# Kernel optimization log

Hardware: AMD Instinct MI355X
Metric: run time of the kernel (lower is better)

## Reference

```python
import jax, jax.numpy as jnp
import numpy as np

N = 50000; E = 800000; F_IN = 165; HID = 32; H1 = 8; H3 = 4; OUT = 2
D1 = H1 * HID  # 256
D3 = H3 * HID  # 128
BN_EPS = 1e-5


def _gat_conv(x, edge_index, W, a_s, a_d, b, heads, add_self_loops):
    n = x.shape[0]
    if add_self_loops:
        loops = jnp.arange(n, dtype=edge_index.dtype)
        edge_index = jnp.concatenate([edge_index, jnp.stack([loops, loops])], axis=1)
    src, dst = edge_index[0], edge_index[1]
    h = (x @ W).reshape(n, heads, -1)                      # [N, H, D]
    a_src = jnp.sum(h * a_s, axis=-1)                      # [N, H]
    a_dst = jnp.sum(h * a_d, axis=-1)                      # [N, H]
    e = jax.nn.leaky_relu(a_src[src] + a_dst[dst], 0.2)    # [E, H] per-edge logits
    m = jax.ops.segment_max(e, dst, num_segments=n)        # segment-softmax over incoming edges
    ex = jnp.exp(e - m[dst])
    den = jax.ops.segment_sum(ex, dst, num_segments=n)
    alpha = ex / (den[dst] + 1e-16)                        # PyG softmax eps
    out = jax.ops.segment_sum(h[src] * alpha[:, :, None], dst, num_segments=n)
    return out.reshape(n, -1) + b                          # concat heads + bias


def _bn(x, g, b, mean, var):  # eval-mode BatchNorm1d
    return (x - mean) * jax.lax.rsqrt(var + BN_EPS) * g + b


def setup_inputs() -> dict:
    key = jax.random.key(0)
    ks = jax.random.split(key, 24)
    rn = lambda i, shape, s=0.05: jax.random.normal(ks[i], shape, dtype=jnp.float32) * s
    d = {}
    d["x"] = jax.random.normal(ks[0], (N, F_IN), dtype=jnp.float32)
    d["edge_index"] = jax.random.randint(ks[1], (2, E), 0, N, dtype=jnp.int32)
    d["W1"] = rn(2, (F_IN, D1)); d["a1s"] = rn(3, (H1, HID)); d["a1d"] = rn(4, (H1, HID))
    d["b1"] = jnp.zeros((D1,), jnp.float32)
    d["g1"] = jnp.ones((D1,), jnp.float32); d["be1"] = jnp.zeros((D1,), jnp.float32)
    d["m1"] = rn(5, (D1,)); d["v1"] = jax.random.uniform(ks[6], (D1,), minval=0.5, maxval=1.5)
    d["W2"] = rn(7, (D1, D1)); d["a2s"] = rn(8, (H1, HID)); d["a2d"] = rn(9, (H1, HID))
    d["b2"] = jnp.zeros((D1,), jnp.float32)
    d["g2"] = jnp.ones((D1,), jnp.float32); d["be2"] = jnp.zeros((D1,), jnp.float32)
    d["m2"] = rn(10, (D1,)); d["v2"] = jax.random.uniform(ks[11], (D1,), minval=0.5, maxval=1.5)
    d["W3"] = rn(12, (D1, D3)); d["a3s"] = rn(13, (H3, HID)); d["a3d"] = rn(14, (H3, HID))
    d["b3"] = jnp.zeros((D3,), jnp.float32)
    d["fcW"] = rn(15, (D3, OUT)); d["fcb"] = jnp.zeros((OUT,), jnp.float32)
    d["skW"] = rn(16, (F_IN, D3)); d["skb"] = jnp.zeros((D3,), jnp.float32)
    d["temp"] = jnp.array(1.0, jnp.float32)
    return d


def reference(x, edge_index, W1, a1s, a1d, b1, g1, be1, m1, v1,
              W2, a2s, a2d, b2, g2, be2, m2, v2,
              W3, a3s, a3d, b3, fcW, fcb, skW, skb, temp):
    x_init = x @ skW + skb                                   # skip Linear
    h = jax.nn.elu(_bn(_gat_conv(x, edge_index, W1, a1s, a1d, b1, H1, False), g1, be1, m1, v1))
    h = jax.nn.elu(_bn(_gat_conv(h, edge_index, W2, a2s, a2d, b2, H1, True), g2, be2, m2, v2) + h)
    h = _gat_conv(h * temp, edge_index, W3, a3s, a3d, b3, H3, True)
    return jax.nn.log_softmax((h + x_init) @ fcW + fcb, axis=1)
```

## Files before the change

### kernel.cpp

```cpp
#include <hip/hip_runtime.h>
#include <hip/hip_bf16.h>
#include <math.h>

#define N_NODES 50000
#define MP      50048
#define N_EDGES 800000
#define F_IN    165
#define KPAD1   192
#define D1      256
#define D3      128
#define CAP     64

typedef __attribute__((ext_vector_type(8))) short short8;
typedef __attribute__((ext_vector_type(4))) float floatx4;
typedef __attribute__((ext_vector_type(2))) float floatx2;

__device__ __forceinline__ float bflo(unsigned u) { return __uint_as_float(u << 16); }
__device__ __forceinline__ float bfhi(unsigned u) { return __uint_as_float(u & 0xffff0000u); }

__device__ __forceinline__ void fma8p(floatx2* a, float wgt, const uint4& v) {
    floatx2 w2; w2.x = wgt; w2.y = wgt;
    floatx2 p;
    p.x = bflo(v.x); p.y = bfhi(v.x); a[0] += w2 * p;
    p.x = bflo(v.y); p.y = bfhi(v.y); a[1] += w2 * p;
    p.x = bflo(v.z); p.y = bfhi(v.z); a[2] += w2 * p;
    p.x = bflo(v.w); p.y = bfhi(v.w); a[3] += w2 * p;
}

#if defined(__has_builtin)
#if __has_builtin(__builtin_amdgcn_global_load_lds)
#define HAS_GLL 1
#endif
#endif

__device__ __forceinline__ void gload16(const void* g, void* lds) {
#ifdef HAS_GLL
    __builtin_amdgcn_global_load_lds(
        (const __attribute__((address_space(1))) unsigned*)g,
        (__attribute__((address_space(3))) unsigned*)lds, 16, 0, 0);
#else
    *(int4*)lds = *(const int4*)g;
#endif
}

__global__ void prep_all(const float* __restrict__ x, __hip_bfloat16* __restrict__ xb,
                         const float* __restrict__ W1, const float* __restrict__ skW,
                         const float* __restrict__ a1s, const float* __restrict__ a1d,
                         __hip_bfloat16* __restrict__ Bt1,
                         const float* __restrict__ W2,
                         const float* __restrict__ a2s, const float* __restrict__ a2d,
                         __hip_bfloat16* __restrict__ Bt2,
                         const float* __restrict__ W3,
                         const float* __restrict__ a3s, const float* __restrict__ a3d,
                         __hip_bfloat16* __restrict__ Bt3)
{
    const long long S0 = (long long)MP * KPAD1;
    const long long S1 = S0 + 256 * KPAD1;
    const long long S2 = S1 + 128 * KPAD1;
    const long long S3 = S2 + 16 * KPAD1;
    const long long S4 = S3 + 256 * D1;
    const long long S5 = S4 + 16 * D1;
    const long long S6 = S5 + 128 * D1;
    const long long S7 = S6 + 8 * D1;
    long long idx = (long long)blockIdx.x * 256 + threadIdx.x;
    if (idx < S0) {
        const int m = idx / KPAD1, k = idx - (long long)m * KPAD1;
        xb[idx] = __float2bfloat16((k < F_IN && m < N_NODES) ? x[(size_t)m * F_IN + k] : 0.f);
    } else if (idx < S1) {
        const long long i = idx - S0;
        const int n = i / KPAD1, k = i - (long long)n * KPAD1;
        Bt1[(size_t)n * KPAD1 + k] = __float2bfloat16((k < F_IN) ? W1[(size_t)k * D1 + n] : 0.f);
    } else if (idx < S2) {
        const long long i = idx - S1;
        const int n = i / KPAD1, k = i - (long long)n * KPAD1;
        Bt1[(size_t)(256 + n) * KPAD1 + k] =
            __float2bfloat16((k < F_IN) ? skW[(size_t)k * D3 + n] : 0.f);
    } else if (idx < S3) {
        const long long i = idx - S2;
        const int r = i / KPAD1, k = i - (long long)r * KPAD1;
        const int hh = r & 7;
        const float* av = (r < 8) ? a1s : a1d;
        float s = 0.f;
        if (k < F_IN)
#pragma unroll
            for (int d = 0; d < 32; ++d) s += W1[(size_t)k * D1 + hh * 32 + d] * av[hh * 32 + d];
        Bt1[(size_t)(384 + r) * KPAD1 + k] = __float2bfloat16(s);
    } else if (idx < S4) {
        const long long i = idx - S3;
        const int n = i / D1, k = i - (long long)n * D1;
        Bt2[(size_t)n * D1 + k] = __float2bfloat16(W2[(size_t)k * D1 + n]);
    } else if (idx < S5) {
        const long long i = idx - S4;
        const int r = i / D1, k = i - (long long)r * D1;
        const int hh = r & 7;
        const float* av = (r < 8) ? a2s : a2d;
        float s = 0.f;
#pragma unroll
        for (int d = 0; d < 32; ++d) s += W2[(size_t)k * D1 + hh * 32 + d] * av[hh * 32 + d];
        Bt2[(size_t)(256 + r) * D1 + k] = __float2bfloat16(s);
    } else if (idx < S6) {
        const long long i = idx - S5;
        const int n = i / D1, k = i - (long long)n * D1;
        Bt3[(size_t)n * D1 + k] = __float2bfloat16(W3[(size_t)k * D3 + n]);
    } else if (idx < S7) {
        const long long i = idx - S6;
        const int r = i / D1, k = i - (long long)r * D1;
        const int hh = r & 3;
        const float* av = (r < 4) ? a3s : a3d;
        float s = 0.f;
#pragma unroll
        for (int d = 0; d < 32; ++d) s += W3[(size_t)k * D3 + hh * 32 + d] * av[hh * 32 + d];
        Bt3[(size_t)(128 + r) * D1 + k] = __float2bfloat16(s);
    }
}

__global__ __launch_bounds__(256) void gemm_bf16(
    const __hip_bfloat16* __restrict__ A, const __hip_bfloat16* __restrict__ Bt,
    const float* __restrict__ alphap,
    __hip_bfloat16* __restrict__ Cb, int Dh,
    __hip_bfloat16* __restrict__ Cx, const float* __restrict__ biasx, int Dx,
    float* __restrict__ asrc, float* __restrict__ adst, int H,
    int M, int Ka)
{
    __shared__ short As[128 * 32];
    __shared__ short Bs[128 * 32];
    const int t  = threadIdx.x;
    const int m0 = blockIdx.x * 128;
    const int n0 = blockIdx.y * 128;
    const int w  = t >> 6, l = t & 63;
    const int wy = w >> 1, wx = w & 1;
    const int lm = l & 15, quad = l >> 4;
    const float alpha = alphap ? alphap[0] : 1.f;
    const int NNlive = Dh + Dx + 2 * H;

    floatx4 acc[4][4] = {};

    const int ch0 = w * 128 + l;
    const int ch1 = ch0 + 64;
    const int r0a = ch0 >> 2, k0a = (ch0 & 3) * 8;
    const int r1a = ch1 >> 2, k1a = (ch1 & 3) * 8;

    for (int k0 = 0; k0 < Ka; k0 += 32) {
        gload16(A  + (size_t)(m0 + r0a) * Ka + k0 + k0a, &As[ch0 * 8]);
        gload16(A  + (size_t)(m0 + r1a) * Ka + k0 + k1a, &As[ch1 * 8]);
        gload16(Bt + (size_t)(n0 + r0a) * Ka + k0 + k0a, &Bs[ch0 * 8]);
        gload16(Bt + (size_t)(n0 + r1a) * Ka + k0 + k1a, &Bs[ch1 * 8]);
        __syncthreads();

        short8 af[4], bf[4];
#pragma unroll
        for (int i = 0; i < 4; ++i) {
            af[i] = *(const short8*)&As[(wy * 64 + i * 16 + lm) * 32 + quad * 8];
            bf[i] = *(const short8*)&Bs[(wx * 64 + i * 16 + lm) * 32 + quad * 8];
        }
#pragma unroll
        for (int mi = 0; mi < 4; ++mi)
#pragma unroll
            for (int ni = 0; ni < 4; ++ni)
                acc[mi][ni] = __builtin_amdgcn_mfma_f32_16x16x32_bf16(
                    af[mi], bf[ni], acc[mi][ni], 0, 0, 0);
        __syncthreads();
    }

#pragma unroll
    for (int mi = 0; mi < 4; ++mi) {
#pragma unroll
        for (int r = 0; r < 4; ++r) {
            const int gm = m0 + wy * 64 + mi * 16 + quad * 4 + r;
            if (gm >= M) continue;
#pragma unroll
            for (int ni = 0; ni < 4; ++ni) {
                const int gn = n0 + wx * 64 + ni * 16 + lm;
                if (gn >= NNlive) continue;
                const float v = acc[mi][ni][r] * alpha;
                if (gn < Dh) {
                    Cb[(size_t)gm * Dh + gn] = __float2bfloat16(v);
                } else if (gn < Dh + Dx) {
                    Cx[(size_t)gm * Dx + gn - Dh] = __float2bfloat16(v + biasx[gn - Dh]);
                } else {
                    const int c = gn - Dh - Dx;
                    if (c < H) asrc[(size_t)gm * H + c] = v;
                    else       adst[(size_t)gm * H + c - H] = v;
                }
            }
        }
    }
}

__global__ void deg_hist(const int* __restrict__ ei, int* __restrict__ deg, int E)
{
    const int e = blockIdx.x * blockDim.x + threadIdx.x;
    if (e < E) atomicAdd(&deg[ei[E + e]], 1);
}

__global__ __launch_bounds__(1024) void scan_rowptr(const int* __restrict__ deg,
                                                    int* __restrict__ rowptr, int n)
{
    __shared__ int sums[1024];
    const int tid = threadIdx.x;
    const int chunk = (n + 1023) / 1024;
    const int lo = tid * chunk;
    const int hi = min(lo + chunk, n);
    int s = 0;
    for (int i = lo; i < hi; ++i) s += deg[i];
    sums[tid] = s;
    __syncthreads();
    for (int off = 1; off < 1024; off <<= 1) {
        int t = 0;
        if (tid >= off) t = sums[tid - off];
        __syncthreads();
        if (tid >= off) sums[tid] += t;
        __syncthreads();
    }
    int run = sums[tid] - s;
    for (int i = lo; i < hi; ++i) { rowptr[i] = run; run += deg[i]; }
    if (lo < n && hi == n) rowptr[n] = run;
}

__global__ void csr_fill(const int* __restrict__ ei, const int* __restrict__ rowptr,
                         int* __restrict__ cursor, int* __restrict__ csr_src, int E)
{
    const int e = blockIdx.x * blockDim.x + threadIdx.x;
    if (e >= E) return;
    const int dst = ei[E + e];
    const int pos = rowptr[dst] + atomicAdd(&cursor[dst], 1);
    csr_src[pos] = ei[e];
}

template <int HSH, int D, int POST>
__global__ __launch_bounds__(256) void gat_gather_v9(
    const __hip_bfloat16* __restrict__ h, const float* __restrict__ asrc,
    const float* __restrict__ adst, const int* __restrict__ rowptr,
    const int* __restrict__ csr_src, int selfloop,
    const float* __restrict__ bias, const float* __restrict__ g,
    const float* __restrict__ be, const float* __restrict__ mean,
    const float* __restrict__ var, const __hip_bfloat16* __restrict__ residB,
    const float* __restrict__ fcW, const float* __restrict__ fcb,
    float* __restrict__ outF, __hip_bfloat16* __restrict__ outB)
{
    constexpr int H    = 1 << HSH;
    constexpr int LPE  = D / 8;
    constexpr int EPW  = 64 / LPE;
    constexpr int SUBS = 64 >> HSH;
    constexpr int MAXJ = CAP / SUBS;

    const int w = threadIdx.x >> 6, l = threadIdx.x & 63;
    const int node = blockIdx.x * 4 + w;

    __shared__ float sW[4][CAP * H];
    __shared__ int   sSrc[4][CAP];

    const int r0  = rowptr[node];
    const int deg = rowptr[node + 1] - r0;
    const int tot = min(deg + selfloop, CAP);

    const int hh  = l & (H - 1);
    const int sub = l >> HSH;
    const float ad = adst[node * H + hh];

    float ex[MAXJ];
    float sum = 0.f;
    {
        int nj = 0;
        for (int e = sub; e < tot; e += SUBS, ++nj) {
            const int s = (e < deg) ? csr_src[r0 + e] : node;
            if (hh == 0) sSrc[w][e] = s;
            float v = asrc[s * H + hh] + ad;
            v = v > 0.f ? v : 0.2f * v;
            ex[nj] = __expf(v);
            sum += ex[nj];
        }
    }
#pragma unroll
    for (int off = H; off < 64; off <<= 1) sum += __shfl_xor(sum, off);
    const float rs = 1.f / (sum + 1e-16f);
    {
        int nj = 0;
        for (int e = sub; e < tot; e += SUBS, ++nj)
            sW[w][e * H + hh] = ex[nj] * rs;
    }

    const int sw   = l / LPE;
    const int lo   = l % LPE;
    const int dimb = lo * 8;
    const int hh2  = dimb >> 5;
    floatx2 a0[4] = {}, a1[4] = {};

    for (int e = sw; e < tot; e += 2 * EPW) {
        const int e2  = e + EPW;
        const bool v2 = e2 < tot;
        const int sa = sSrc[w][e];
        const int sb = v2 ? sSrc[w][e2] : node;
        const float wa = sW[w][e * H + hh2];
        const float wb = v2 ? sW[w][e2 * H + hh2] : 0.f;
        const uint4 qa = *(const uint4*)&h[(size_t)sa * D + dimb];
        const uint4 qb = *(const uint4*)&h[(size_t)sb * D + dimb];
        fma8p(a0, wa, qa);
        fma8p(a1, wb, qb);
    }
    float acc[8];
#pragma unroll
    for (int v = 0; v < 4; ++v) {
        const floatx2 s2v = a0[v] + a1[v];
        acc[v * 2] = s2v.x; acc[v * 2 + 1] = s2v.y;
    }
#pragma unroll
    for (int off = LPE; off < 64; off <<= 1)
#pragma unroll
        for (int v = 0; v < 8; ++v) acc[v] += __shfl_xor(acc[v], off);

    if (POST == 3) {
        float v0 = 0.f, v1 = 0.f;
        if (l < LPE) {
            const uint4 rv = *(const uint4*)&residB[(size_t)node * D + dimb];
            const float rr[8] = {bflo(rv.x), bfhi(rv.x), bflo(rv.y), bfhi(rv.y),
                                 bflo(rv.z), bfhi(rv.z), bflo(rv.w), bfhi(rv.w)};
#pragma unroll
            for (int v = 0; v < 8; ++v) {
                const float val = acc[v] + bias[dimb + v] + rr[v];
                v0 += val * fcW[(dimb + v) * 2 + 0];
                v1 += val * fcW[(dimb + v) * 2 + 1];
            }
        }
#pragma unroll
        for (int off = 1; off < LPE; off <<= 1) {
            v0 += __shfl_xor(v0, off);
            v1 += __shfl_xor(v1, off);
        }
        if (l == 0) {
            const float l0 = v0 + fcb[0], l1 = v1 + fcb[1];
            const float m2 = fmaxf(l0, l1);
            const float lse = m2 + logf(__expf(l0 - m2) + __expf(l1 - m2));
            outF[node * 2 + 0] = l0 - lse;
            outF[node * 2 + 1] = l1 - lse;
        }
    } else {
        if (l < LPE) {
            float rr[8] = {};
            if (POST == 2) {
                const uint4 rv = *(const uint4*)&residB[(size_t)node * D + dimb];
                rr[0] = bflo(rv.x); rr[1] = bfhi(rv.x);
                rr[2] = bflo(rv.y); rr[3] = bfhi(rv.y);
                rr[4] = bflo(rv.z); rr[5] = bfhi(rv.z);
                rr[6] = bflo(rv.w); rr[7] = bfhi(rv.w);
            }
            __hip_bfloat16 rb[8];
#pragma unroll
            for (int v = 0; v < 8; ++v) {
                const int f = dimb + v;
                float vv = acc[v] + bias[f];
                vv = (vv - mean[f]) * rsqrtf(var[f] + 1e-5f) * g[f] + be[f];
                if (POST == 2) vv += rr[v];
                vv = vv > 0.f ? vv : (__expf(vv) - 1.f);
                rb[v] = __float2bfloat16(vv);
            }
            *(uint4*)&outB[(size_t)node * D + dimb] = *(uint4*)&rb[0];
        }
    }
}

extern "C" void kernel_launch(void* const* d_in, const int* in_sizes, int n_in,
                              void* d_out, int out_size, void* d_ws, size_t ws_size,
                              hipStream_t stream)
{
    const float* x    = (const float*)d_in[0];
    const int*   ei   = (const int*)  d_in[1];
    const float* W1   = (const float*)d_in[2];
    const float* a1s  = (const float*)d_in[3];
    const float* a1d  = (const float*)d_in[4];
    const float* b1   = (const float*)d_in[5];
    const float* g1   = (const float*)d_in[6];
    const float* be1  = (const float*)d_in[7];
    const float* m1   = (const float*)d_in[8];
    const float* v1   = (const float*)d_in[9];
    const float* W2   = (const float*)d_in[10];
    const float* a2s  = (const float*)d_in[11];
    const float* a2d  = (const float*)d_in[12];
    const float* b2   = (const float*)d_in[13];
    const float* g2   = (const float*)d_in[14];
    const float* be2  = (const float*)d_in[15];
    const float* m2   = (const float*)d_in[16];
    const float* v2   = (const float*)d_in[17];
    const float* W3   = (const float*)d_in[18];
    const float* a3s  = (const float*)d_in[19];
    const float* a3d  = (const float*)d_in[20];
    const float* b3   = (const float*)d_in[21];
    const float* fcW  = (const float*)d_in[22];
    const float* fcb  = (const float*)d_in[23];
    const float* skW  = (const float*)d_in[24];
    const float* skb  = (const float*)d_in[25];
    const float* temp = (const float*)d_in[26];

    float* out = (float*)d_out;

    const int N = N_NODES, E = N_EDGES;

    float* ws = (float*)d_ws;
    size_t o = 0;
    float* asrc  = ws + o;  o += (size_t)N * 8;
    float* adst  = ws + o;  o += (size_t)N * 8;
    int* rowptr  = (int*)(ws + o);  o += N + 1;
    o = (o + 3) & ~(size_t)3;
    int* csr_src = (int*)(ws + o);  o += E;
    o = (o + 3) & ~(size_t)3;
    __hip_bfloat16* xb     = (__hip_bfloat16*)(ws + o); o += (size_t)MP * KPAD1 / 2;
    __hip_bfloat16* bufCb  = (__hip_bfloat16*)(ws + o); o += (size_t)MP * D1 / 2;
    __hip_bfloat16* hb     = (__hip_bfloat16*)(ws + o); o += (size_t)N * D1 / 2;
    __hip_bfloat16* xinitB = (__hip_bfloat16*)(ws + o); o += (size_t)N * D3 / 2;
    __hip_bfloat16* Bt1    = (__hip_bfloat16*)(ws + o); o += (size_t)512 * KPAD1 / 2;
    __hip_bfloat16* Bt2    = (__hip_bfloat16*)(ws + o); o += (size_t)384 * D1 / 2;
    __hip_bfloat16* Bt3    = (__hip_bfloat16*)(ws + o); o += (size_t)256 * D1 / 2;
    int* deg    = (int*)hb;
    int* cursor = deg + N;

    const int MT128 = MP / 128;

    hipMemsetAsync(deg, 0, (size_t)2 * N * sizeof(int), stream);
    deg_hist<<<(E + 255) / 256, 256, 0, stream>>>(ei, deg, E);
    scan_rowptr<<<1, 1024, 0, stream>>>(deg, rowptr, N);
    csr_fill<<<(E + 255) / 256, 256, 0, stream>>>(ei, rowptr, cursor, csr_src, E);

    {
        const long long tote = (long long)MP * KPAD1 + (256 + 128 + 16) * (long long)KPAD1 +
                               (256 + 16 + 128 + 8) * (long long)D1;
        prep_all<<<(tote + 255) / 256, 256, 0, stream>>>(
            x, xb, W1, skW, a1s, a1d, Bt1, W2, a2s, a2d, Bt2, W3, a3s, a3d, Bt3);
    }

    gemm_bf16<<<dim3(MT128, 4), 256, 0, stream>>>(xb, Bt1, nullptr,
                                                  hb, D1, xinitB, skb, D3,
                                                  asrc, adst, 8, N, KPAD1);
    gat_gather_v9<3, D1, 1><<<N / 4, 256, 0, stream>>>(hb, asrc, adst, rowptr, csr_src, 0,
                                                       b1, g1, be1, m1, v1, nullptr, nullptr, nullptr,
                                                       nullptr, bufCb);

    gemm_bf16<<<dim3(MT128, 3), 256, 0, stream>>>(bufCb, Bt2, nullptr,
                                                  hb, D1, nullptr, nullptr, 0,
                                                  asrc, adst, 8, N, D1);
    gat_gather_v9<3, D1, 2><<<N / 4, 256, 0, stream>>>(hb, asrc, adst, rowptr, csr_src, 1,
                                                       b2, g2, be2, m2, v2, bufCb, nullptr, nullptr,
                                                       nullptr, bufCb);

    gemm_bf16<<<dim3(MT128, 2), 256, 0, stream>>>(bufCb, Bt3, temp,
                                                  hb, D3, nullptr, nullptr, 0,
                                                  asrc, adst, 4, N, D1);
    gat_gather_v9<2, D3, 3><<<N / 4, 256, 0, stream>>>(hb, asrc, adst, rowptr, csr_src, 1,
                                                       b3, nullptr, nullptr, nullptr, nullptr, xinitB,
                                                       fcW, fcb, out, nullptr);

    (void)in_sizes; (void)n_in; (void)out_size; (void)ws_size;
}
```

Baseline: 617.3 us.

## Fuse degree histogram into prep kernel and loop N-tiles inside GEMM blocks

```diff
diff --git a/kernel.cpp b/kernel.cpp
--- a/kernel.cpp
+++ b/kernel.cpp
@@ -43,17 +43,24 @@
 #endif
 }
 
-__global__ void prep_all(const float* __restrict__ x, __hip_bfloat16* __restrict__ xb,
-                         const float* __restrict__ W1, const float* __restrict__ skW,
-                         const float* __restrict__ a1s, const float* __restrict__ a1d,
-                         __hip_bfloat16* __restrict__ Bt1,
-                         const float* __restrict__ W2,
-                         const float* __restrict__ a2s, const float* __restrict__ a2d,
-                         __hip_bfloat16* __restrict__ Bt2,
-                         const float* __restrict__ W3,
-                         const float* __restrict__ a3s, const float* __restrict__ a3d,
-                         __hip_bfloat16* __restrict__ Bt3)
-{
+__global__ void prep_hist(const int* __restrict__ ei, int* __restrict__ deg,
+                          const float* __restrict__ x, __hip_bfloat16* __restrict__ xb,
+                          const float* __restrict__ W1, const float* __restrict__ skW,
+                          const float* __restrict__ a1s, const float* __restrict__ a1d,
+                          __hip_bfloat16* __restrict__ Bt1,
+                          const float* __restrict__ W2,
+                          const float* __restrict__ a2s, const float* __restrict__ a2d,
+                          __hip_bfloat16* __restrict__ Bt2,
+                          const float* __restrict__ W3,
+                          const float* __restrict__ a3s, const float* __restrict__ a3d,
+                          __hip_bfloat16* __restrict__ Bt3)
+{
+    long long gidx = (long long)blockIdx.x * 256 + threadIdx.x;
+    if (gidx < N_EDGES) {
+        atomicAdd(&deg[ei[N_EDGES + gidx]], 1);
+        return;
+    }
+    long long idx = gidx - N_EDGES;
     const long long S0 = (long long)MP * KPAD1;
     const long long S1 = S0 + 256 * KPAD1;
     const long long S2 = S1 + 128 * KPAD1;
@@ -62,7 +69,6 @@
     const long long S5 = S4 + 16 * D1;
     const long long S6 = S5 + 128 * D1;
     const long long S7 = S6 + 8 * D1;
-    long long idx = (long long)blockIdx.x * 256 + threadIdx.x;
     if (idx < S0) {
         const int m = idx / KPAD1, k = idx - (long long)m * KPAD1;
         xb[idx] = __float2bfloat16((k < F_IN && m < N_NODES) ? x[(size_t)m * F_IN + k] : 0.f);
@@ -120,77 +126,73 @@
     __hip_bfloat16* __restrict__ Cb, int Dh,
     __hip_bfloat16* __restrict__ Cx, const float* __restrict__ biasx, int Dx,
     float* __restrict__ asrc, float* __restrict__ adst, int H,
-    int M, int Ka)
+    int M, int Ka, int NT)
 {
     __shared__ short As[128 * 32];
     __shared__ short Bs[128 * 32];
     const int t  = threadIdx.x;
     const int m0 = blockIdx.x * 128;
-    const int n0 = blockIdx.y * 128;
     const int w  = t >> 6, l = t & 63;
     const int wy = w >> 1, wx = w & 1;
     const int lm = l & 15, quad = l >> 4;
     const float alpha = alphap ? alphap[0] : 1.f;
     const int NNlive = Dh + Dx + 2 * H;
 
-    floatx4 acc[4][4] = {};
-
     const int ch0 = w * 128 + l;
     const int ch1 = ch0 + 64;
     const int r0a = ch0 >> 2, k0a = (ch0 & 3) * 8;
     const int r1a = ch1 >> 2, k1a = (ch1 & 3) * 8;
 
-    for (int k0 = 0; k0 < Ka; k0 += 32) {
-        gload16(A  + (size_t)(m0 + r0a) * Ka + k0 + k0a, &As[ch0 * 8]);
-        gload16(A  + (size_t)(m0 + r1a) * Ka + k0 + k1a, &As[ch1 * 8]);
-        gload16(Bt + (size_t)(n0 + r0a) * Ka + k0 + k0a, &Bs[ch0 * 8]);
-        gload16(Bt + (size_t)(n0 + r1a) * Ka + k0 + k1a, &Bs[ch1 * 8]);
-        __syncthreads();
-
-        short8 af[4], bf[4];
-#pragma unroll
-        for (int i = 0; i < 4; ++i) {
-            af[i] = *(const short8*)&As[(wy * 64 + i * 16 + lm) * 32 + quad * 8];
-            bf[i] = *(const short8*)&Bs[(wx * 64 + i * 16 + lm) * 32 + quad * 8];
-        }
-#pragma unroll
-        for (int mi = 0; mi < 4; ++mi)
-#pragma unroll
-            for (int ni = 0; ni < 4; ++ni)
-                acc[mi][ni] = __builtin_amdgcn_mfma_f32_16x16x32_bf16(
-                    af[mi], bf[ni], acc[mi][ni], 0, 0, 0);
-        __syncthreads();
-    }
-
-#pragma unroll
-    for (int mi = 0; mi < 4; ++mi) {
-#pragma unroll
-        for (int r = 0; r < 4; ++r) {
-            const int gm = m0 + wy * 64 + mi * 16 + quad * 4 + r;
-            if (gm >= M) continue;
-#pragma unroll
-            for (int ni = 0; ni < 4; ++ni) {
-                const int gn = n0 + wx * 64 + ni * 16 + lm;
-                if (gn >= NNlive) continue;
-                const float v = acc[mi][ni][r] * alpha;
-                if (gn < Dh) {
-                    Cb[(size_t)gm * Dh + gn] = __float2bfloat16(v);
-                } else if (gn < Dh + Dx) {
-                    Cx[(size_t)gm * Dx + gn - Dh] = __float2bfloat16(v + biasx[gn - Dh]);
-                } else {
-                    const int c = gn - Dh - Dx;
-                    if (c < H) asrc[(size_t)gm * H + c] = v;
-                    else       adst[(size_t)gm * H + c - H] = v;
+    for (int nt = 0; nt < NT; ++nt) {
+        const int n0 = nt * 128;
+        floatx4 acc[4][4] = {};
+
+        for (int k0 = 0; k0 < Ka; k0 += 32) {
+            gload16(A  + (size_t)(m0 + r0a) * Ka + k0 + k0a, &As[ch0 * 8]);
+            gload16(A  + (size_t)(m0 + r1a) * Ka + k0 + k1a, &As[ch1 * 8]);
+            gload16(Bt + (size_t)(n0 + r0a) * Ka + k0 + k0a, &Bs[ch0 * 8]);
+            gload16(Bt + (size_t)(n0 + r1a) * Ka + k0 + k1a, &Bs[ch1 * 8]);
+            __syncthreads();
+
+            short8 af[4], bf[4];
+#pragma unroll
+            for (int i = 0; i < 4; ++i) {
+                af[i] = *(const short8*)&As[(wy * 64 + i * 16 + lm) * 32 + quad * 8];
+                bf[i] = *(const short8*)&Bs[(wx * 64 + i * 16 + lm) * 32 + quad * 8];
+            }
+#pragma unroll
+            for (int mi = 0; mi < 4; ++mi)
+#pragma unroll
+                for (int ni = 0; ni < 4; ++ni)
+                    acc[mi][ni] = __builtin_amdgcn_mfma_f32_16x16x32_bf16(
+                        af[mi], bf[ni], acc[mi][ni], 0, 0, 0);
+            __syncthreads();
+        }
+
+#pragma unroll
+        for (int mi = 0; mi < 4; ++mi) {
+#pragma unroll
+            for (int r = 0; r < 4; ++r) {
+                const int gm = m0 + wy * 64 + mi * 16 + quad * 4 + r;
+                if (gm >= M) continue;
+#pragma unroll
+                for (int ni = 0; ni < 4; ++ni) {
+                    const int gn = n0 + wx * 64 + ni * 16 + lm;
+                    if (gn >= NNlive) continue;
+                    const float v = acc[mi][ni][r] * alpha;
+                    if (gn < Dh) {
+                        Cb[(size_t)gm * Dh + gn] = __float2bfloat16(v);
+                    } else if (gn < Dh + Dx) {
+                        Cx[(size_t)gm * Dx + gn - Dh] = __float2bfloat16(v + biasx[gn - Dh]);
+                    } else {
+                        const int c = gn - Dh - Dx;
+                        if (c < H) asrc[(size_t)gm * H + c] = v;
+                        else       adst[(size_t)gm * H + c - H] = v;
+                    }
                 }
             }
         }
     }
-}
-
-__global__ void deg_hist(const int* __restrict__ ei, int* __restrict__ deg, int E)
-{
-    const int e = blockIdx.x * blockDim.x + threadIdx.x;
-    if (e < E) atomicAdd(&deg[ei[E + e]], 1);
 }
 
 __global__ __launch_bounds__(1024) void scan_rowptr(const int* __restrict__ deg,
@@ -416,34 +418,33 @@
     const int MT128 = MP / 128;
 
     hipMemsetAsync(deg, 0, (size_t)2 * N * sizeof(int), stream);
-    deg_hist<<<(E + 255) / 256, 256, 0, stream>>>(ei, deg, E);
+    {
+        const long long tote = (long long)E + (long long)MP * KPAD1 +
+                               (256 + 128 + 16) * (long long)KPAD1 +
+                               (256 + 16 + 128 + 8) * (long long)D1;
+        prep_hist<<<(tote + 255) / 256, 256, 0, stream>>>(
+            ei, deg, x, xb, W1, skW, a1s, a1d, Bt1, W2, a2s, a2d, Bt2, W3, a3s, a3d, Bt3);
+    }
     scan_rowptr<<<1, 1024, 0, stream>>>(deg, rowptr, N);
     csr_fill<<<(E + 255) / 256, 256, 0, stream>>>(ei, rowptr, cursor, csr_src, E);
 
-    {
-        const long long tote = (long long)MP * KPAD1 + (256 + 128 + 16) * (long long)KPAD1 +
-                               (256 + 16 + 128 + 8) * (long long)D1;
-        prep_all<<<(tote + 255) / 256, 256, 0, stream>>>(
-            x, xb, W1, skW, a1s, a1d, Bt1, W2, a2s, a2d, Bt2, W3, a3s, a3d, Bt3);
-    }
-
-    gemm_bf16<<<dim3(MT128, 4), 256, 0, stream>>>(xb, Bt1, nullptr,
-                                                  hb, D1, xinitB, skb, D3,
-                                                  asrc, adst, 8, N, KPAD1);
+    gemm_bf16<<<MT128, 256, 0, stream>>>(xb, Bt1, nullptr,
+                                         hb, D1, xinitB, skb, D3,
+                                         asrc, adst, 8, N, KPAD1, 4);
     gat_gather_v9<3, D1, 1><<<N / 4, 256, 0, stream>>>(hb, asrc, adst, rowptr, csr_src, 0,
                                                        b1, g1, be1, m1, v1, nullptr, nullptr, nullptr,
                                                        nullptr, bufCb);
 
-    gemm_bf16<<<dim3(MT128, 3), 256, 0, stream>>>(bufCb, Bt2, nullptr,
-                                                  hb, D1, nullptr, nullptr, 0,
-                                                  asrc, adst, 8, N, D1);
+    gemm_bf16<<<MT128, 256, 0, stream>>>(bufCb, Bt2, nullptr,
+                                         hb, D1, nullptr, nullptr, 0,
+                                         asrc, adst, 8, N, D1, 3);
     gat_gather_v9<3, D1, 2><<<N / 4, 256, 0, stream>>>(hb, asrc, adst, rowptr, csr_src, 1,
                                                        b2, g2, be2, m2, v2, bufCb, nullptr, nullptr,
                                                        nullptr, bufCb);
 
-    gemm_bf16<<<dim3(MT128, 2), 256, 0, stream>>>(bufCb, Bt3, temp,
-                                                  hb, D3, nullptr, nullptr, 0,
-                                                  asrc, adst, 4, N, D1);
+    gemm_bf16<<<MT128, 256, 0, stream>>>(bufCb, Bt3, temp,
+                                         hb, D3, nullptr, nullptr, 0,
+                                         asrc, adst, 4, N, D1, 2);
     gat_gather_v9<2, D3, 3><<<N / 4, 256, 0, stream>>>(hb, asrc, adst, rowptr, csr_src, 1,
                                                        b3, nullptr, nullptr, nullptr, nullptr, xinitB,
                                                        fcW, fcb, out, nullptr);
```

Result: slower. 687.8 us (+11.4%).
